# Performance work log

Measured on AMD Instinct MI355X. Metric: run time of the kernel, lower is better.

The kernel has to match this reference:

```python
import jax, jax.numpy as jnp
import numpy as np
import math

HIDDEN = 2048
NUM_HEADS = 32
HEAD_DIM = 64
WINDOW = 1024
GLOBAL_HEADS = 2
LOCAL_HEADS = NUM_HEADS - GLOBAL_HEADS
ROPE_BASE = 10000.0


def rotate_half(x):
    x1, x2 = jnp.split(x, 2, axis=-1)
    return jnp.concatenate([-x2, x1], axis=-1)


def rope_cos_sin(positions, dim):
    inv_freq = 1.0 / (ROPE_BASE ** (jnp.arange(0, dim, 2, dtype=jnp.float32) / dim))
    freqs = positions[:, None].astype(jnp.float32) * inv_freq[None, :]  # [L, dim/2]
    emb = jnp.concatenate([freqs, freqs], axis=-1)  # [L, dim]
    return jnp.cos(emb)[None, None], jnp.sin(emb)[None, None]  # [1,1,L,dim]


def apply_rope(q, k, q_pos, k_pos):
    cos_q, sin_q = rope_cos_sin(q_pos, q.shape[-1])
    cos_k, sin_k = rope_cos_sin(k_pos, k.shape[-1])
    return q * cos_q + rotate_half(q) * sin_q, k * cos_k + rotate_half(k) * sin_k


def sliding_window_attention_blockwise(q, k, v, window_size):
    # faithful to torch _blockwise_attention (causal=True, no attention_mask)
    B, H, L, D = q.shape
    block = min(window_size, 1024)
    scale = 1.0 / math.sqrt(D)
    outs = []
    for start in range(0, L, block):
        end = min(start + block, L)
        ks = max(0, start - window_size // 2)
        ke = end  # causal clamp: k_end = min(end + window//2, end)
        qb = q[:, :, start:end]
        kb = k[:, :, ks:ke]
        vb = v[:, :, ks:ke]
        s = jnp.einsum('bhqd,bhkd->bhqk', qb, kb) * scale
        qi = jnp.arange(start, end)[:, None]
        ki = jnp.arange(ks, ke)[None, :]
        s = jnp.where(qi >= ki, s, -jnp.inf)
        a = jax.nn.softmax(s, axis=-1)
        outs.append(jnp.einsum('bhqk,bhkd->bhqd', a, vb))
    return jnp.concatenate(outs, axis=2)


def global_attention(q, k, v):
    B, H, L, D = q.shape
    scale = 1.0 / math.sqrt(D)
    s = jnp.einsum('bhqd,bhkd->bhqk', q, k) * scale
    causal = jnp.tril(jnp.ones((L, L), dtype=bool))
    s = jnp.where(causal[None, None], s, -jnp.inf)
    a = jax.nn.softmax(s, axis=-1)
    return jnp.einsum('bhqk,bhkd->bhqd', a, v)


def setup_inputs() -> dict:
    key = jax.random.key(0)
    k1, k2, k3, k4, k5, k6 = jax.random.split(key, 6)
    B, L = 2, 4096
    P = NUM_HEADS * HEAD_DIM
    return {
        'hidden_states': jax.random.normal(k1, (B, L, HIDDEN), dtype=jnp.float32),
        'Wq': jax.random.normal(k2, (P, HIDDEN), dtype=jnp.float32) * 0.02,
        'Wk': jax.random.normal(k3, (P, HIDDEN), dtype=jnp.float32) * 0.02,
        'Wv': jax.random.normal(k4, (P, HIDDEN), dtype=jnp.float32) * 0.02,
        'Wo': jax.random.normal(k5, (HIDDEN, P), dtype=jnp.float32) * 0.02,
        'bo': jax.random.normal(k6, (HIDDEN,), dtype=jnp.float32) * 0.02,
    }


def reference(hidden_states, Wq, Wk, Wv, Wo, bo):
    B, L, _ = hidden_states.shape
    q = jnp.einsum('blh,ph->blp', hidden_states, Wq).reshape(B, L, NUM_HEADS, HEAD_DIM).transpose(0, 2, 1, 3)
    k = jnp.einsum('blh,ph->blp', hidden_states, Wk).reshape(B, L, NUM_HEADS, HEAD_DIM).transpose(0, 2, 1, 3)
    v = jnp.einsum('blh,ph->blp', hidden_states, Wv).reshape(B, L, NUM_HEADS, HEAD_DIM).transpose(0, 2, 1, 3)
    pos = jnp.arange(L)
    q, k = apply_rope(q, k, pos, pos)
    # first LOCAL_HEADS heads use sliding-window, last GLOBAL_HEADS use global attention
    ql, qg = q[:, :LOCAL_HEADS], q[:, LOCAL_HEADS:]
    kl, kg = k[:, :LOCAL_HEADS], k[:, LOCAL_HEADS:]
    vl, vg = v[:, :LOCAL_HEADS], v[:, LOCAL_HEADS:]
    out_local = sliding_window_attention_blockwise(ql, kl, vl, WINDOW)
    out_global = global_attention(qg, kg, vg)
    out = jnp.concatenate([out_local, out_global], axis=1)  # [B,H,L,D]
    out = out.transpose(0, 2, 1, 3).reshape(B, L, NUM_HEADS * HEAD_DIM)
    return jnp.einsum('blp,hp->blh', out, Wo) + bo
```

## Files before the change

kernel.cpp:

```cpp
#include <hip/hip_runtime.h>
#include <hip/hip_bf16.h>
#include <stdint.h>

#define HID 2048
#define SEQ 4096
#define BATCH 2
#define NH 32
#define HD 64
#define ROWS (BATCH*SEQ)
#define LOCAL_H 30
#define LOG2E 1.4426950408889634f
#define NT 32

typedef __attribute__((ext_vector_type(4))) float f32x4;
typedef __attribute__((ext_vector_type(16))) float f32x16;
typedef __attribute__((ext_vector_type(8))) short s16x8;
typedef __attribute__((ext_vector_type(4))) unsigned int u32x4;

__device__ __forceinline__ void g2l16(const void* g, void* l) {
  __builtin_amdgcn_global_load_lds((__attribute__((address_space(1))) void*)(g),
                                   (__attribute__((address_space(3))) void*)(l), 16, 0, 0);
}

__device__ __forceinline__ unsigned pk2(float a, float b) {
  union { __hip_bfloat16 h; unsigned short u; } x, y;
  x.h = __float2bfloat16(a); y.h = __float2bfloat16(b);
  return ((unsigned)y.u << 16) | x.u;
}

__device__ __forceinline__ unsigned cvtpk(float lo, float hi) {
  unsigned d;
  asm("v_cvt_pk_bf16_f32 %0, %1, %2" : "=v"(d) : "v"(lo), "v"(hi));
  return d;
}

__device__ __forceinline__ void pl32swap(unsigned &a, unsigned &b) {
  asm volatile("v_permlane32_swap_b32 %0, %1" : "+v"(a), "+v"(b));
}

__device__ const unsigned char Gq40[40] = {0,1,2,3, 4,4,5,5,6,6,7,7,
  8,8,8,9,9,9,10,10,10,11,11,11, 12,12,12,12,13,13,13,13,14,14,14,14,15,15,15,15};
__device__ const unsigned char Gs40[40] = {0,0,0,0, 0,1,0,1,0,1,0,1,
  0,1,2,0,1,2,0,1,2,0,1,2, 0,1,2,3,0,1,2,3,0,1,2,3,0,1,2,3};
__device__ const unsigned char PG16[16] = {0,0,0,0, 0,2,4,6, 8,11,14,17, 20,24,28,32};
__device__ const unsigned char Lq22[22] = {6,6,7,7,10,10,11,11,14,14,15,15, 0,1,2,3,4,5,8,9,12,13};
__device__ const unsigned char Ls22[22] = {0,1,0,1,0,1,0,1,0,1,0,1, 0,0,0,0,0,0,0,0,0,0};
__device__ const unsigned char QT6[6]   = {6,7,10,11,14,15};
__device__ const unsigned char PG12[12] = {0,2,4,6,8,11,14,17,20,24,28,32};

__global__ __launch_bounds__(256) void castk(const float* __restrict__ s,
                                             __hip_bfloat16* __restrict__ d, int n8) {
  int i = blockIdx.x * 256 + threadIdx.x;
  if (i >= n8) return;
  const f32x4* sp = (const f32x4*)(s) + (size_t)i * 2;
  f32x4 a = sp[0], b = sp[1];
  __hip_bfloat16 t[8];
#pragma unroll
  for (int j = 0; j < 4; j++) { t[j] = __float2bfloat16(a[j]); t[j+4] = __float2bfloat16(b[j]); }
  *(s16x8*)(d + (size_t)i * 8) = *(const s16x8*)t;
}

__global__ __launch_bounds__(256) void castw(const float* __restrict__ w0,
                                             const float* __restrict__ w1,
                                             const float* __restrict__ w2,
                                             const float* __restrict__ w3,
                                             __hip_bfloat16* __restrict__ dbase) {
  const float* s = (blockIdx.y == 0) ? w0 : (blockIdx.y == 1) ? w1 : (blockIdx.y == 2) ? w2 : w3;
  __hip_bfloat16* d = dbase + (size_t)blockIdx.y * HID * HID;
  int i = blockIdx.x * 256 + threadIdx.x;
  const f32x4* sp = (const f32x4*)(s) + (size_t)i * 2;
  f32x4 a = sp[0], b = sp[1];
  __hip_bfloat16 t[8];
#pragma unroll
  for (int j = 0; j < 4; j++) { t[j] = __float2bfloat16(a[j]); t[j+4] = __float2bfloat16(b[j]); }
  *(s16x8*)(d + (size_t)i * 8) = *(const s16x8*)t;
}

template<int OP>
__global__ __launch_bounds__(512, 2) void gemm256(const __hip_bfloat16* __restrict__ A,
                                                  const __hip_bfloat16* __restrict__ Wbase,
                                                  const float* __restrict__ bias,
                                                  __hip_bfloat16* __restrict__ Qr,
                                                  __hip_bfloat16* __restrict__ Kr,
                                                  __hip_bfloat16* __restrict__ Vt,
                                                  float* __restrict__ Oout) {
  __shared__ __hip_bfloat16 lds[2][4][128 * 64];
  const int tid = threadIdx.x;
  const int lane = tid & 63, wv = tid >> 6;
  const int wm = wv >> 2, wn = wv & 3;
  const int g = lane >> 4, ln = lane & 15;
  const int m0 = blockIdx.y * 256;

  int which, n0;
  const __hip_bfloat16* W;
  if constexpr (OP == 0) {
    which = blockIdx.x >> 3; n0 = (blockIdx.x & 7) * 256;
    W = Wbase + (size_t)which * HID * HID;
  } else {
    which = 3; n0 = blockIdx.x * 256; W = Wbase;
  }

  const int srow = tid >> 3, sslot = tid & 7;
  const int scolE = (sslot ^ (srow & 7)) * 8;
  const int srow2 = (512 + tid) >> 3;
  const int scolE2 = (sslot ^ (srow2 & 7)) * 8;

#define STAGE(srcbase, kt, region)                                              \
  {                                                                             \
    g2l16((srcbase) + (size_t)(srow) * HID + (kt) + scolE,                      \
          (void*)(&lds[0][0][0] + (region) * 8192 + wv * 512));                 \
    g2l16((srcbase) + (size_t)(srow2) * HID + (kt) + scolE2,                    \
          (void*)(&lds[0][0][0] + (region) * 8192 + 4096 + wv * 512));          \
  }

  f32x4 acc[8][4];
#pragma unroll
  for (int i = 0; i < 8; i++)
#pragma unroll
    for (int j = 0; j < 4; j++) acc[i][j] = (f32x4)0.f;

  STAGE(A + (size_t)m0 * HID,           0, 0);
  STAGE(W + (size_t)n0 * HID,           0, 2);
  STAGE(W + (size_t)(n0 + 128) * HID,   0, 3);
  STAGE(A + (size_t)(m0 + 128) * HID,   0, 1);

  for (int t = 0; t < NT; ++t) {
    const int buf = t & 1, nbuf = buf ^ 1;
    const int ktn = (t + 1) * 64;
    const bool pre = (t + 1 < NT);
    const __hip_bfloat16* Bh = &lds[buf][2 + (wn >> 1)][0];
    s16x8 bfv[4][2];

#pragma unroll
    for (int mi = 0; mi < 2; mi++) {
      if (pre) {
        if (mi == 0) { STAGE(A + (size_t)m0 * HID,         ktn, nbuf * 4 + 0) }
        else         { STAGE(W + (size_t)(n0 + 128) * HID, ktn, nbuf * 4 + 3) }
        if (mi == 0) { asm volatile("s_waitcnt vmcnt(4)" ::: "memory"); }
        else         { asm volatile("s_waitcnt vmcnt(6)" ::: "memory"); }
      } else if (mi == 0) {
        asm volatile("s_waitcnt vmcnt(0)" ::: "memory");
      }
      __builtin_amdgcn_sched_barrier(0);
      __builtin_amdgcn_s_barrier();
      __builtin_amdgcn_sched_barrier(0);

      const __hip_bfloat16* Ah = &lds[buf][mi][0];
      s16x8 af[4][2];
#pragma unroll
      for (int st = 0; st < 4; st++) {
        int row = wm * 64 + st * 16 + ln;
#pragma unroll
        for (int ks = 0; ks < 2; ks++)
          af[st][ks] = *(const s16x8*)(Ah + row * 64 + (((ks * 4 + g) ^ (row & 7)) * 8));
      }
      if (mi == 0) {
#pragma unroll
        for (int nf = 0; nf < 4; nf++) {
          int row = (wn & 1) * 64 + nf * 16 + ln;
#pragma unroll
          for (int ks = 0; ks < 2; ks++)
            bfv[nf][ks] = *(const s16x8*)(Bh + row * 64 + (((ks * 4 + g) ^ (row & 7)) * 8));
        }
      }
#pragma unroll
      for (int ni = 0; ni < 2; ni++) {
        if (pre && ni == 1) {
          if (mi == 0) { STAGE(W + (size_t)n0 * HID,         ktn, nbuf * 4 + 2) }
          else         { STAGE(A + (size_t)(m0 + 128) * HID, ktn, nbuf * 4 + 1) }
        }
        __builtin_amdgcn_s_setprio(1);
#pragma unroll
        for (int st = 0; st < 4; st++)
#pragma unroll
          for (int st2 = 0; st2 < 2; st2++)
#pragma unroll
            for (int ks = 0; ks < 2; ks++)
              acc[mi * 4 + st][ni * 2 + st2] =
                __builtin_amdgcn_mfma_f32_16x16x32_bf16(af[st][ks], bfv[ni * 2 + st2][ks],
                                                        acc[mi * 4 + st][ni * 2 + st2], 0, 0, 0);
        __builtin_amdgcn_s_setprio(0);
      }
    }
  }
#undef STAGE

  const int n0c = n0 + (wn >> 1) * 128 + (wn & 1) * 64;
  if constexpr (OP == 1) {
#pragma unroll
    for (int am = 0; am < 8; am++) {
#pragma unroll
      for (int r = 0; r < 4; r++) {
        int grow = m0 + (am >> 2) * 128 + wm * 64 + (am & 3) * 16 + g * 4 + r;
        float* o = Oout + (size_t)grow * HID + n0c;
#pragma unroll
        for (int j = 0; j < 4; j++)
          o[j * 16 + ln] = acc[am][j][r] + bias[n0c + j * 16 + ln];
      }
    }
  } else if (which == 2) {
#pragma unroll
    for (int am = 0; am < 8; am++) {
      int growb = m0 + (am >> 2) * 128 + wm * 64 + (am & 3) * 16 + g * 4;
      int b = growb >> 12, l0 = growb & (SEQ - 1);
#pragma unroll
      for (int j = 0; j < 4; j++) {
        int c = n0c + j * 16 + ln;
        __hip_bfloat16* vp = Vt + ((size_t)(b * NH + (c >> 6)) * HD + (c & 63)) * SEQ + l0;
        *(unsigned*)(vp)     = pk2(acc[am][j][0], acc[am][j][1]);
        *(unsigned*)(vp + 2) = pk2(acc[am][j][2], acc[am][j][3]);
      }
    }
  } else {
    __hip_bfloat16* outp = (which == 0) ? Qr : Kr;
    int h = n0c >> 6;
#pragma unroll
    for (int am = 0; am < 8; am++) {
      int growb = m0 + (am >> 2) * 128 + wm * 64 + (am & 3) * 16 + g * 4;
      int b = growb >> 12;
#pragma unroll
      for (int r = 0; r < 4; r++) {
        int l = (growb & (SEQ - 1)) + r;
        __hip_bfloat16* o = outp + ((size_t)(b * NH + h) * SEQ + l) * HD;
#pragma unroll
        for (int j = 0; j < 2; j++) {
          int d = j * 16 + ln;
          float x1 = acc[am][j][r], x2 = acc[am][j + 2][r];
          float ang = (float)l * exp2f((float)d * -0.41524101186091903f);
          float sn, cs;
          __sincosf(ang, &sn, &cs);
          float o1 = x1 * cs - x2 * sn;
          float o2 = x2 * cs + x1 * sn;
          if (which == 0) { o1 *= 0.125f * LOG2E; o2 *= 0.125f * LOG2E; }
          o[d]      = __float2bfloat16(o1);
          o[d + 32] = __float2bfloat16(o2);
        }
      }
    }
  }
}

__global__ __launch_bounds__(512, 4) void flash(const __hip_bfloat16* __restrict__ Q,
                                                const __hip_bfloat16* __restrict__ Kk,
                                                const __hip_bfloat16* __restrict__ Vt,
                                                __hip_bfloat16* __restrict__ attn,
                                                __hip_bfloat16* __restrict__ PO,
                                                float* __restrict__ PM,
                                                float* __restrict__ PL) {
  __shared__ __hip_bfloat16 Ks[2][64 * 64];
  __shared__ __hip_bfloat16 Vs[2][64 * 64];

  int bi = blockIdx.x;
  int b, h, qtl, seg, pidx;
  if (bi < 160) {
    int gidx = bi / 40, r = bi % 40;
    qtl = Gq40[r]; seg = Gs40[r];
    int nseg = (qtl >> 2) + 1;
    b = gidx >> 1; h = 30 + (gidx & 1);
    pidx = (nseg > 1) ? (720 + gidx * 36 + PG16[qtl] + seg) : -1;
  } else {
    int li = bi - 160;
    int lidx = li / 22, r = li % 22;
    qtl = Lq22[r]; seg = Ls22[r];
    b = lidx / 30; h = lidx % 30;
    pidx = (r < 12) ? (lidx * 12 + r) : -1;
  }
  const int bhid = b * NH + h;
  const int q0 = qtl * 256;
  int ks0t = 0;
  if (h < LOCAL_H) { int gq = qtl >> 2; ks0t = gq ? gq * 1024 - 512 : 0; }
  const int kstart = ks0t + seg * 1024;
  const int kend_t = q0 + 256;
  const int kend_s = (kend_t < kstart + 1024) ? kend_t : kstart + 1024;
  const int nch = (kend_s - kstart) >> 6;

  const int tid = threadIdx.x, lane = tid & 63, wv = tid >> 6;
  const int ln32 = lane & 31, hi = lane >> 5;
  const int qw0 = q0 + wv * 32;
  const int qg = qw0 + ln32;

  const __hip_bfloat16* qb = Q + ((size_t)bhid * SEQ + qg) * HD + hi * 8;
  s16x8 qf[4];
#pragma unroll
  for (int tt = 0; tt < 4; tt++) qf[tt] = *(const s16x8*)(qb + tt * 16);

  float mrow = -3.0e38f, lrow = 0.f;
  f32x16 o0 = (f32x16)0.f, o1 = (f32x16)0.f;

  const int srow = tid >> 3, sslot = tid & 7;
  const int scolE = (sslot ^ (srow & 7) ^ ((srow >> 1) & 4)) * 8;
  const int sxor = (ln32 & 7) ^ ((ln32 >> 1) & 4);

#define STAGEKV(bb, kc)                                                                   \
  {                                                                                       \
    g2l16(Kk + ((size_t)bhid * SEQ + (kc) + srow) * HD + scolE, (void*)(&Ks[bb][0] + wv * 512)); \
    g2l16(Vt + ((size_t)bhid * HD + srow) * SEQ + (kc) + scolE, (void*)(&Vs[bb][0] + wv * 512)); \
  }

  STAGEKV(0, kstart)

  int cur = 0;
  for (int ci = 0; ci < nch; ci++) {
    int kc = kstart + ci * 64;
    if (ci + 1 < nch) {
      STAGEKV(cur ^ 1, kc + 64)
      asm volatile("s_waitcnt vmcnt(2)" ::: "memory");
    } else {
      asm volatile("s_waitcnt vmcnt(0)" ::: "memory");
    }
    __builtin_amdgcn_s_barrier();
    __builtin_amdgcn_sched_barrier(0);

    if (kc <= qw0 + 31) {
      const __hip_bfloat16* Kc = &Ks[cur][0];
      const __hip_bfloat16* Vc = &Vs[cur][0];

      f32x16 s0 = (f32x16)0.f, s1 = (f32x16)0.f;
      __builtin_amdgcn_s_setprio(1);
#pragma unroll
      for (int tt = 0; tt < 4; tt++) {
        int sl = ((2 * tt + hi) ^ sxor) * 8;
        s16x8 ka = *(const s16x8*)(Kc + ln32 * 64 + sl);
        s0 = __builtin_amdgcn_mfma_f32_32x32x16_bf16(ka, qf[tt], s0, 0, 0, 0);
        s16x8 kb = *(const s16x8*)(Kc + (32 + ln32) * 64 + sl);
        s1 = __builtin_amdgcn_mfma_f32_32x32x16_bf16(kb, qf[tt], s1, 0, 0, 0);
      }
      __builtin_amdgcn_s_setprio(0);

      if (kc + 63 > qw0) {
#pragma unroll
        for (int r = 0; r < 16; r++) {
          int kv0 = kc + (r & 3) + 8 * (r >> 2) + 4 * hi;
          if (kv0 > qg) s0[r] = -1.0e30f;
          if (kv0 + 32 > qg) s1[r] = -1.0e30f;
        }
      }

      float pm = fmaxf(s0[0], s1[0]);
#pragma unroll
      for (int r = 1; r < 16; r++) pm = fmaxf(pm, fmaxf(s0[r], s1[r]));
      pm = fmaxf(pm, __shfl_xor(pm, 32));
      bool resc = !__all(pm <= mrow + 8.0f);
      float mu = resc ? fmaxf(mrow, pm) : mrow;
      float ps = 0.f;
#pragma unroll
      for (int r = 0; r < 16; r++) { float p = exp2f(s0[r] - mu); s0[r] = p; ps += p; }
#pragma unroll
      for (int r = 0; r < 16; r++) { float p = exp2f(s1[r] - mu); s1[r] = p; ps += p; }
      ps += __shfl_xor(ps, 32);
      if (resc) {
        float corr = exp2f(mrow - mu);
        lrow = lrow * corr + ps;
        mrow = mu;
#pragma unroll
        for (int r = 0; r < 16; r++) { o0[r] *= corr; o1[r] *= corr; }
      } else {
        lrow += ps;
      }

      s16x8 pfr[4];
#pragma unroll
      for (int fb = 0; fb < 4; fb++) {
        const f32x16& tile = (fb < 2) ? s0 : s1;
        const int base = (fb & 1) * 8;
        unsigned X = cvtpk(tile[base + 0], tile[base + 1]);
        unsigned Y = cvtpk(tile[base + 2], tile[base + 3]);
        unsigned Z = cvtpk(tile[base + 4], tile[base + 5]);
        unsigned Wd = cvtpk(tile[base + 6], tile[base + 7]);
        pl32swap(X, Z);
        pl32swap(Y, Wd);
        u32x4 wq; wq.x = X; wq.y = Y; wq.z = Z; wq.w = Wd;
        pfr[fb] = __builtin_bit_cast(s16x8, wq);
      }

      __builtin_amdgcn_s_setprio(1);
#pragma unroll
      for (int ss = 0; ss < 4; ss++) {
        int sl = ((2 * ss + hi) ^ sxor) * 8;
        s16x8 va = *(const s16x8*)(Vc + ln32 * 64 + sl);
        o0 = __builtin_amdgcn_mfma_f32_32x32x16_bf16(va, pfr[ss], o0, 0, 0, 0);
        s16x8 vb = *(const s16x8*)(Vc + (32 + ln32) * 64 + sl);
        o1 = __builtin_amdgcn_mfma_f32_32x32x16_bf16(vb, pfr[ss], o1, 0, 0, 0);
      }
      __builtin_amdgcn_s_setprio(0);
    }

    __builtin_amdgcn_sched_barrier(0);
    asm volatile("s_waitcnt lgkmcnt(0)" ::: "memory");
    __builtin_amdgcn_s_barrier();
    cur ^= 1;
  }
#undef STAGEKV

  if (pidx < 0) {
    float linv = 1.0f / lrow;
    int orow = b * SEQ + qg;
    __hip_bfloat16* ob = attn + (size_t)orow * HID + h * HD;
#pragma unroll
    for (int rp = 0; rp < 16; rp += 2) {
      int d0 = (rp & 3) + 8 * (rp >> 2) + 4 * hi;
      *(unsigned*)(ob + d0)      = pk2(o0[rp] * linv, o0[rp + 1] * linv);
      *(unsigned*)(ob + 32 + d0) = pk2(o1[rp] * linv, o1[rp + 1] * linv);
    }
  } else {
    int tq = wv * 32 + ln32;
    __hip_bfloat16* pob = PO + ((size_t)pidx * 256 + tq) * 64;
#pragma unroll
    for (int rp = 0; rp < 16; rp += 2) {
      int d0 = (rp & 3) + 8 * (rp >> 2) + 4 * hi;
      *(unsigned*)(pob + d0)      = pk2(o0[rp], o0[rp + 1]);
      *(unsigned*)(pob + 32 + d0) = pk2(o1[rp], o1[rp + 1]);
    }
    if (hi == 0) {
      PM[pidx * 256 + tq] = mrow;
      PL[pidx * 256 + tq] = lrow;
    }
  }
}

__global__ __launch_bounds__(256) void combine(const __hip_bfloat16* __restrict__ PO,
                                               const float* __restrict__ PM,
                                               const float* __restrict__ PL,
                                               __hip_bfloat16* __restrict__ attn) {
  int bi = blockIdx.x;
  int b, h, qtl, ns, pbase;
  if (bi < 360) {
    int lidx = bi / 6, j2 = bi % 6;
    qtl = QT6[j2]; ns = 2; pbase = lidx * 12 + j2 * 2;
    b = lidx / 30; h = lidx % 30;
  } else {
    int gi = bi - 360;
    int gidx = gi / 12, j2 = gi % 12;
    qtl = 4 + j2; ns = (qtl >> 2) + 1;
    pbase = 720 + gidx * 36 + PG12[j2];
    b = gidx >> 1; h = 30 + (gidx & 1);
  }
  int tq = threadIdx.x;
  float m = -3.0e38f;
  for (int s = 0; s < ns; s++) m = fmaxf(m, PM[(pbase + s) * 256 + tq]);
  float wsum = 0.f;
  float oacc[64];
#pragma unroll
  for (int d = 0; d < 64; d++) oacc[d] = 0.f;
  for (int s = 0; s < ns; s++) {
    float w = exp2f(PM[(pbase + s) * 256 + tq] - m);
    wsum += w * PL[(pbase + s) * 256 + tq];
    const s16x8* po = (const s16x8*)(PO + ((size_t)(pbase + s) * 256 + tq) * 64);
#pragma unroll
    for (int u = 0; u < 8; u++) {
      s16x8 v = po[u];
#pragma unroll
      for (int e = 0; e < 8; e++) {
        union { unsigned uu; float f; } cv;
        cv.uu = ((unsigned)(unsigned short)v[e]) << 16;
        oacc[u * 8 + e] += w * cv.f;
      }
    }
  }
  float inv = 1.0f / wsum;
  __hip_bfloat16* ob = attn + ((size_t)(b * SEQ + qtl * 256 + tq)) * HID + h * HD;
#pragma unroll
  for (int d = 0; d < 64; d += 2)
    *(unsigned*)(ob + d) = pk2(oacc[d] * inv, oacc[d + 1] * inv);
}

extern "C" void kernel_launch(void* const* d_in, const int* in_sizes, int n_in,
                              void* d_out, int out_size, void* d_ws, size_t ws_size,
                              hipStream_t stream) {
  (void)in_sizes; (void)n_in; (void)out_size; (void)ws_size;
  const float* hid = (const float*)d_in[0];
  const float* Wq  = (const float*)d_in[1];
  const float* Wk  = (const float*)d_in[2];
  const float* Wv  = (const float*)d_in[3];
  const float* Wo  = (const float*)d_in[4];
  const float* bo  = (const float*)d_in[5];

  char* ws = (char*)d_ws;
  size_t off = 0;
  __hip_bfloat16* hidB = (__hip_bfloat16*)(ws + off); off += (size_t)ROWS * HID * 2;
  __hip_bfloat16* WqB  = (__hip_bfloat16*)(ws + off); off += (size_t)HID * HID * 2 * 4;
  __hip_bfloat16* WoB  = WqB + (size_t)3 * HID * HID;
  __hip_bfloat16* Qr   = (__hip_bfloat16*)(ws + off); off += (size_t)ROWS * HID * 2;
  __hip_bfloat16* Kr   = (__hip_bfloat16*)(ws + off); off += (size_t)ROWS * HID * 2;
  __hip_bfloat16* Vt   = (__hip_bfloat16*)(ws + off); off += (size_t)ROWS * HID * 2;
  __hip_bfloat16* PO   = (__hip_bfloat16*)(ws + off); off += (size_t)864 * 256 * 64 * 2;
  float* PM            = (float*)(ws + off);          off += (size_t)864 * 256 * 4;
  float* PL            = (float*)(ws + off);          off += (size_t)864 * 256 * 4;
  __hip_bfloat16* attn = hidB;

  castk<<<(ROWS * HID / 8 + 255) / 256, 256, 0, stream>>>(hid, hidB, ROWS * HID / 8);
  castw<<<dim3(HID * HID / 8 / 256, 4), 256, 0, stream>>>(Wq, Wk, Wv, Wo, WqB);

  gemm256<0><<<dim3(24, 32), 512, 0, stream>>>(hidB, WqB, nullptr, Qr, Kr, Vt, nullptr);

  flash<<<1480, 512, 0, stream>>>(Qr, Kr, Vt, attn, PO, PM, PL);
  combine<<<408, 256, 0, stream>>>(PO, PM, PL, attn);

  gemm256<1><<<dim3(8, 32), 512, 0, stream>>>(attn, WoB, bo, nullptr, nullptr, nullptr, (float*)d_out);
}
```

Baseline: 457.4 us.

## Load GEMM B fragments directly to registers and remap blocks for XCD locality

The GEMM kernel no longer stages the weight (B) tile through LDS. Each wave loads its B fragments straight into registers with global_load_dwordx4, double-buffered across K tiles, which halves LDS use and drops the B LDS reads. A 1D grid with an XCD-aware block index remap is added so that neighbouring tiles sharing data run on the same XCD for L2 reuse. The trade-off is higher register pressure (the launch bounds minimum-occupancy hint is removed) and redundant global loads of B across the two wm waves.

```diff
diff --git a/kernel.cpp b/kernel.cpp
--- a/kernel.cpp
+++ b/kernel.cpp
@@ -20,6 +20,12 @@
 __device__ __forceinline__ void g2l16(const void* g, void* l) {
   __builtin_amdgcn_global_load_lds((__attribute__((address_space(1))) void*)(g),
                                    (__attribute__((address_space(3))) void*)(l), 16, 0, 0);
+}
+
+__device__ __forceinline__ u32x4 gload16(const void* p) {
+  u32x4 d;
+  asm volatile("global_load_dwordx4 %0, %1, off" : "=v"(d) : "v"(p) : "memory");
+  return d;
 }
 
 __device__ __forceinline__ unsigned pk2(float a, float b) {
@@ -77,27 +83,33 @@
 }
 
 template<int OP>
-__global__ __launch_bounds__(512, 2) void gemm256(const __hip_bfloat16* __restrict__ A,
-                                                  const __hip_bfloat16* __restrict__ Wbase,
-                                                  const float* __restrict__ bias,
-                                                  __hip_bfloat16* __restrict__ Qr,
-                                                  __hip_bfloat16* __restrict__ Kr,
-                                                  __hip_bfloat16* __restrict__ Vt,
-                                                  float* __restrict__ Oout) {
-  __shared__ __hip_bfloat16 lds[2][4][128 * 64];
+__global__ __launch_bounds__(512) void gemm256(const __hip_bfloat16* __restrict__ A,
+                                               const __hip_bfloat16* __restrict__ Wbase,
+                                               const float* __restrict__ bias,
+                                               __hip_bfloat16* __restrict__ Qr,
+                                               __hip_bfloat16* __restrict__ Kr,
+                                               __hip_bfloat16* __restrict__ Vt,
+                                               float* __restrict__ Oout) {
+  __shared__ __hip_bfloat16 lds[2][2][128 * 64];
   const int tid = threadIdx.x;
   const int lane = tid & 63, wv = tid >> 6;
   const int wm = wv >> 2, wn = wv & 3;
   const int g = lane >> 4, ln = lane & 15;
-  const int m0 = blockIdx.y * 256;
-
-  int which, n0;
+
+  int which, n0, m0;
   const __hip_bfloat16* W;
-  if constexpr (OP == 0) {
-    which = blockIdx.x >> 3; n0 = (blockIdx.x & 7) * 256;
-    W = Wbase + (size_t)which * HID * HID;
-  } else {
-    which = 3; n0 = blockIdx.x * 256; W = Wbase;
+  {
+    int bid = blockIdx.x;
+    if constexpr (OP == 0) {
+      int wgid = (bid & 7) * 96 + (bid >> 3);
+      int xidx = wgid >> 5, midx = wgid & 31;
+      which = xidx >> 3; n0 = (xidx & 7) * 256; m0 = midx * 256;
+      W = Wbase + (size_t)which * HID * HID;
+    } else {
+      int wgid = (bid & 7) * 32 + (bid >> 3);
+      which = 3; n0 = (wgid >> 5) * 256; m0 = (wgid & 31) * 256;
+      W = Wbase;
+    }
   }
 
   const int srow = tid >> 3, sslot = tid & 7;
@@ -105,12 +117,24 @@
   const int srow2 = (512 + tid) >> 3;
   const int scolE2 = (sslot ^ (srow2 & 7)) * 8;
 
-#define STAGE(srcbase, kt, region)                                              \
-  {                                                                             \
-    g2l16((srcbase) + (size_t)(srow) * HID + (kt) + scolE,                      \
-          (void*)(&lds[0][0][0] + (region) * 8192 + wv * 512));                 \
-    g2l16((srcbase) + (size_t)(srow2) * HID + (kt) + scolE2,                    \
-          (void*)(&lds[0][0][0] + (region) * 8192 + 4096 + wv * 512));          \
+#define STAGE_A(mi_, kt, bufb)                                                   \
+  {                                                                              \
+    const __hip_bfloat16* sb = A + (size_t)(m0 + (mi_) * 128) * HID;             \
+    g2l16(sb + (size_t)srow * HID + (kt) + scolE,                                \
+          (void*)(&lds[0][0][0] + ((bufb) * 2 + (mi_)) * 8192 + wv * 512));      \
+    g2l16(sb + (size_t)srow2 * HID + (kt) + scolE2,                              \
+          (void*)(&lds[0][0][0] + ((bufb) * 2 + (mi_)) * 8192 + 4096 + wv * 512));\
+  }
+
+  const __hip_bfloat16* wrow = W + (size_t)(n0 + (wn >> 1) * 128 + (wn & 1) * 64 + ln) * HID
+                                 + g * 8;
+#define LOADB(dst, kt)                                                           \
+  {                                                                              \
+    _Pragma("unroll")                                                            \
+    for (int nf = 0; nf < 4; nf++)                                               \
+      _Pragma("unroll")                                                          \
+      for (int ks = 0; ks < 2; ks++)                                             \
+        dst[nf * 2 + ks] = gload16(wrow + (size_t)nf * 16 * HID + (kt) + ks * 32);\
   }
 
   f32x4 acc[8][4];
@@ -119,71 +143,67 @@
 #pragma unroll
     for (int j = 0; j < 4; j++) acc[i][j] = (f32x4)0.f;
 
-  STAGE(A + (size_t)m0 * HID,           0, 0);
-  STAGE(W + (size_t)n0 * HID,           0, 2);
-  STAGE(W + (size_t)(n0 + 128) * HID,   0, 3);
-  STAGE(A + (size_t)(m0 + 128) * HID,   0, 1);
-
-  for (int t = 0; t < NT; ++t) {
-    const int buf = t & 1, nbuf = buf ^ 1;
-    const int ktn = (t + 1) * 64;
-    const bool pre = (t + 1 < NT);
-    const __hip_bfloat16* Bh = &lds[buf][2 + (wn >> 1)][0];
-    s16x8 bfv[4][2];
-
-#pragma unroll
-    for (int mi = 0; mi < 2; mi++) {
-      if (pre) {
-        if (mi == 0) { STAGE(A + (size_t)m0 * HID,         ktn, nbuf * 4 + 0) }
-        else         { STAGE(W + (size_t)(n0 + 128) * HID, ktn, nbuf * 4 + 3) }
-        if (mi == 0) { asm volatile("s_waitcnt vmcnt(4)" ::: "memory"); }
-        else         { asm volatile("s_waitcnt vmcnt(6)" ::: "memory"); }
-      } else if (mi == 0) {
-        asm volatile("s_waitcnt vmcnt(0)" ::: "memory");
-      }
-      __builtin_amdgcn_sched_barrier(0);
-      __builtin_amdgcn_s_barrier();
-      __builtin_amdgcn_sched_barrier(0);
-
-      const __hip_bfloat16* Ah = &lds[buf][mi][0];
-      s16x8 af[4][2];
-#pragma unroll
-      for (int st = 0; st < 4; st++) {
-        int row = wm * 64 + st * 16 + ln;
-#pragma unroll
-        for (int ks = 0; ks < 2; ks++)
-          af[st][ks] = *(const s16x8*)(Ah + row * 64 + (((ks * 4 + g) ^ (row & 7)) * 8));
-      }
-      if (mi == 0) {
-#pragma unroll
-        for (int nf = 0; nf < 4; nf++) {
-          int row = (wn & 1) * 64 + nf * 16 + ln;
-#pragma unroll
-          for (int ks = 0; ks < 2; ks++)
-            bfv[nf][ks] = *(const s16x8*)(Bh + row * 64 + (((ks * 4 + g) ^ (row & 7)) * 8));
-        }
-      }
-#pragma unroll
-      for (int ni = 0; ni < 2; ni++) {
-        if (pre && ni == 1) {
-          if (mi == 0) { STAGE(W + (size_t)n0 * HID,         ktn, nbuf * 4 + 2) }
-          else         { STAGE(A + (size_t)(m0 + 128) * HID, ktn, nbuf * 4 + 1) }
-        }
-        __builtin_amdgcn_s_setprio(1);
-#pragma unroll
-        for (int st = 0; st < 4; st++)
-#pragma unroll
-          for (int st2 = 0; st2 < 2; st2++)
-#pragma unroll
-            for (int ks = 0; ks < 2; ks++)
-              acc[mi * 4 + st][ni * 2 + st2] =
-                __builtin_amdgcn_mfma_f32_16x16x32_bf16(af[st][ks], bfv[ni * 2 + st2][ks],
-                                                        acc[mi * 4 + st][ni * 2 + st2], 0, 0, 0);
-        __builtin_amdgcn_s_setprio(0);
-      }
-    }
-  }
-#undef STAGE
+  u32x4 bA[8], bB[8];
+
+  LOADB(bA, 0)
+  STAGE_A(0, 0, 0)
+  STAGE_A(1, 0, 0)
+  asm volatile("s_waitcnt vmcnt(0)" ::: "memory");
+  __builtin_amdgcn_sched_barrier(0);
+  __builtin_amdgcn_s_barrier();
+
+#define TILE(t_, BCUR, BNXT)                                                     \
+  {                                                                              \
+    const int buf = (t_) & 1, nbuf = buf ^ 1;                                    \
+    const int ktn = ((t_) + 1) * 64;                                             \
+    const bool pre = ((t_) + 1 < NT);                                            \
+    _Pragma("unroll")                                                            \
+    for (int mi = 0; mi < 2; mi++) {                                             \
+      if (mi == 0) {                                                             \
+        if (pre) { STAGE_A(0, ktn, nbuf)                                         \
+                   asm volatile("s_waitcnt vmcnt(2)" ::: "memory"); }            \
+        else     { asm volatile("s_waitcnt vmcnt(0)" ::: "memory"); }            \
+        __builtin_amdgcn_sched_barrier(0);                                       \
+        __builtin_amdgcn_s_barrier();                                            \
+        __builtin_amdgcn_sched_barrier(0);                                       \
+      } else {                                                                   \
+        if (pre) { STAGE_A(1, ktn, nbuf)                                         \
+                   LOADB(BNXT, ktn) }                                            \
+        __builtin_amdgcn_sched_barrier(0);                                       \
+        __builtin_amdgcn_s_barrier();                                            \
+        __builtin_amdgcn_sched_barrier(0);                                       \
+      }                                                                          \
+      const __hip_bfloat16* Ah = &lds[buf][mi][0];                               \
+      s16x8 af[4][2];                                                            \
+      _Pragma("unroll")                                                          \
+      for (int st = 0; st < 4; st++) {                                           \
+        int row = wm * 64 + st * 16 + ln;                                        \
+        _Pragma("unroll")                                                        \
+        for (int ks = 0; ks < 2; ks++)                                           \
+          af[st][ks] = *(const s16x8*)(Ah + row * 64 + (((ks * 4 + g) ^ (row & 7)) * 8)); \
+      }                                                                          \
+      __builtin_amdgcn_s_setprio(1);                                             \
+      _Pragma("unroll")                                                          \
+      for (int st = 0; st < 4; st++)                                             \
+        _Pragma("unroll")                                                        \
+        for (int nf = 0; nf < 4; nf++)                                           \
+          _Pragma("unroll")                                                      \
+          for (int ks = 0; ks < 2; ks++)                                         \
+            acc[mi * 4 + st][nf] =                                               \
+              __builtin_amdgcn_mfma_f32_16x16x32_bf16(af[st][ks],                \
+                  __builtin_bit_cast(s16x8, BCUR[nf * 2 + ks]),                  \
+                  acc[mi * 4 + st][nf], 0, 0, 0);                                \
+      __builtin_amdgcn_s_setprio(0);                                             \
+    }                                                                            \
+  }
+
+  for (int t = 0; t < NT; t += 2) {
+    TILE(t,     bA, bB)
+    TILE(t + 1, bB, bA)
+  }
+#undef TILE
+#undef LOADB
+#undef STAGE_A
 
   const int n0c = n0 + (wn >> 1) * 128 + (wn & 1) * 64;
   if constexpr (OP == 1) {
@@ -491,10 +511,10 @@
   castk<<<(ROWS * HID / 8 + 255) / 256, 256, 0, stream>>>(hid, hidB, ROWS * HID / 8);
   castw<<<dim3(HID * HID / 8 / 256, 4), 256, 0, stream>>>(Wq, Wk, Wv, Wo, WqB);
 
-  gemm256<0><<<dim3(24, 32), 512, 0, stream>>>(hidB, WqB, nullptr, Qr, Kr, Vt, nullptr);
+  gemm256<0><<<768, 512, 0, stream>>>(hidB, WqB, nullptr, Qr, Kr, Vt, nullptr);
 
   flash<<<1480, 512, 0, stream>>>(Qr, Kr, Vt, attn, PO, PM, PL);
   combine<<<408, 256, 0, stream>>>(PO, PM, PL, attn);
 
-  gemm256<1><<<dim3(8, 32), 512, 0, stream>>>(attn, WoB, bo, nullptr, nullptr, nullptr, (float*)d_out);
-}
+  gemm256<1><<<256, 512, 0, stream>>>(attn, WoB, bo, nullptr, nullptr, nullptr, (float*)d_out);
+}
```

New measurement: 578.1 us. +26.4%, slower.
